# Kernel tuning notes

Measured on AMD Instinct MI355X. Metric: run time of the kernel, lower is better.

Reference implementation:

```python
import jax, jax.numpy as jnp
import numpy as np

B, P, G, CIN, COUT, WD, K3 = 4, 32768, 64, 128, 128, 512, 27
N = B * P


def _build_kernel_map(rng):
    # random sparse occupancy per batch instance on a G^3 grid
    flat = np.stack([rng.choice(G ** 3, size=P, replace=False) for _ in range(B)])  # [B,P]
    b = np.repeat(np.arange(B), P).astype(np.int64)
    f = flat.reshape(-1).astype(np.int64)
    x = f // (G * G); y = (f // G) % G; z = f % G
    keys = b * (G ** 3) + f
    order = np.argsort(keys); skeys = keys[order]
    offsets = [(dx, dy, dz) for dx in (-1, 0, 1) for dy in (-1, 0, 1) for dz in (-1, 0, 1)]
    in_idx = np.full((K3, N), N, np.int32)   # N is a dummy (zero-feature) row
    out_idx = np.full((K3, N), N, np.int32)  # N is a dummy (discarded) output row
    for k, (dx, dy, dz) in enumerate(offsets):
        nx, ny, nz = x + dx, y + dy, z + dz
        inb = (nx >= 0) & (nx < G) & (ny >= 0) & (ny < G) & (nz >= 0) & (nz < G)
        nkey = b * (G ** 3) + (nx * G + ny) * G + nz
        pos = np.clip(np.searchsorted(skeys, nkey), 0, N - 1)
        found = inb & (skeys[pos] == nkey)
        cnt = int(found.sum())
        in_idx[k, :cnt] = order[pos[found]]
        out_idx[k, :cnt] = np.nonzero(found)[0]
    return b.astype(np.int32), in_idx, out_idx


def setup_inputs() -> dict:
    rng = np.random.default_rng(0)
    batch_idx, in_idx, out_idx = _build_kernel_map(rng)
    key = jax.random.key(0)
    k1, k2, k3, k4 = jax.random.split(key, 4)
    return {
        "x_feat": jax.random.normal(k1, (N, CIN), jnp.float32),
        "w": jax.random.normal(k2, (B, WD), jnp.float32),
        "affine_weight": jax.random.normal(k3, (CIN, WD), jnp.float32),
        "affine_bias": jnp.ones((CIN,), jnp.float32),  # bias_init=1
        "conv_weight": jax.random.normal(k4, (COUT, CIN, 3, 3, 3), jnp.float32),
        "conv_bias": jnp.zeros((COUT,), jnp.float32),
        "magnitude_ema": jnp.ones((), jnp.float32),
        "batch_idx": jnp.asarray(batch_idx),
        "in_idx": jnp.asarray(in_idx),
        "out_idx": jnp.asarray(out_idx),
    }


def reference(x_feat, w, affine_weight, affine_bias, conv_weight, conv_bias,
              magnitude_ema, batch_idx, in_idx, out_idx):
    n, cin = x_feat.shape
    cout = conv_weight.shape[0]
    # affine: FullyConnectedLayer with weight_gain = 1/sqrt(in_features), bias_init=1
    styles = w @ (affine_weight * (1.0 / np.sqrt(affine_weight.shape[1]))).T + affine_bias  # [B,Cin]
    # demodulate pre-normalization
    wn = conv_weight * jax.lax.rsqrt(jnp.mean(jnp.square(conv_weight), axis=(1, 2, 3, 4), keepdims=True))
    sn = styles * jax.lax.rsqrt(jnp.mean(jnp.square(styles)))
    sw = wn[None] * sn[:, None, :, None, None, None]              # [B,Cout,Cin,3,3,3]
    dcoefs = jax.lax.rsqrt(jnp.sum(jnp.square(sw), axis=(2, 3, 4, 5)) + 1e-8)  # [B,Cout]
    # non-fused modconv: per-point style modulation (index_select by batch column)
    xmod = x_feat * sn[batch_idx]                                 # [N,Cin]
    xpad = jnp.concatenate([xmod, jnp.zeros((1, cin), xmod.dtype)], axis=0)
    # sparse conv: gather -> GEMM -> scatter-add per kernel offset
    wk = jnp.transpose(wn.reshape(cout, cin, K3), (2, 1, 0))      # [27,Cin,Cout]
    out = jnp.zeros((n + 1, cout), x_feat.dtype)
    for k in range(K3):
        out = out.at[out_idx[k]].add(xpad[in_idx[k]] @ wk[k])
    out = out[:n]
    out = out * dcoefs[batch_idx]                                 # demodulation per point
    out = out * jax.lax.rsqrt(magnitude_ema)                      # input_gain
    # fused bias + leaky relu + gain + clamp
    out = out + conv_bias
    out = jnp.where(out < 0, 0.2 * out, out) * np.sqrt(2.0)
    return jnp.clip(out, -256.0, 256.0)
```

## Files before the change

### kernel.cpp

```cpp
#include <hip/hip_runtime.h>
#include <stdint.h>

#define NPTS 131072
#define CINC 128
#define COUTC 128
#define WDIM 512
#define K3 27

typedef float f32x4 __attribute__((ext_vector_type(4)));
typedef __bf16 bf16x8 __attribute__((ext_vector_type(8)));

#define GLOAD_LDS16(g, l) \
  __builtin_amdgcn_global_load_lds((const __attribute__((address_space(1))) void*)(g), \
                                   (__attribute__((address_space(3))) void*)(l), 16, 0, 0)

__device__ __forceinline__ unsigned short f2bf(float x){
  union { float f; uint32_t u; } v; v.f = x;
  uint32_t u = v.u;
  uint32_t r = (u + 0x7fffu + ((u >> 16) & 1u)) >> 16;
  return (unsigned short)r;
}

__global__ void k_styles_dot(const float* __restrict__ w, const float* __restrict__ aw,
                             const float* __restrict__ ab, float* __restrict__ styles){
  int wave = threadIdx.x >> 6, lane = threadIdx.x & 63;
  int blk = blockIdx.x * 4 + wave;
  int b = blk >> 7, c = blk & 127;
  const float4* wr = (const float4*)(w + b * WDIM);
  const float4* ar = (const float4*)(aw + c * WDIM);
  float4 w0 = wr[lane * 2], w1 = wr[lane * 2 + 1];
  float4 a0 = ar[lane * 2], a1 = ar[lane * 2 + 1];
  float s = w0.x * a0.x + w0.y * a0.y + w0.z * a0.z + w0.w * a0.w
          + w1.x * a1.x + w1.y * a1.y + w1.z * a1.z + w1.w * a1.w;
  for (int off = 32; off > 0; off >>= 1) s += __shfl_down(s, off, 64);
  if (lane == 0) styles[blk] = s * 0.04419417382415922f + ab[c];
}

__global__ void k_snorm(const float* __restrict__ styles, float* __restrict__ sn){
  __shared__ float red[512];
  int t = threadIdx.x;
  float s = styles[t];
  red[t] = s * s;
  __syncthreads();
  for (int off = 256; off > 0; off >>= 1){
    if (t < off) red[t] += red[t + off];
    __syncthreads();
  }
  sn[t] = s * rsqrtf(red[0] * (1.0f / 512.0f));
}

__global__ void k_prep_w(const float* __restrict__ cw, float* __restrict__ wnorm,
                         float* __restrict__ vmat, unsigned short* __restrict__ bpack){
  __shared__ float red[128];
  int co = blockIdx.x, cin = threadIdx.x;
  const float* p = cw + co * 3456 + cin * 27;
  float r[27];
  float v = 0.f;
  #pragma unroll
  for (int k = 0; k < 27; k++){ r[k] = p[k]; v += r[k] * r[k]; }
  vmat[co * 128 + cin] = v;
  red[cin] = v;
  __syncthreads();
  for (int off = 64; off > 0; off >>= 1){
    if (cin < off) red[cin] += red[cin + off];
    __syncthreads();
  }
  float wn_s = rsqrtf(red[0] * (1.0f / 3456.0f));
  if (cin == 0) wnorm[co] = wn_s;
  int grp = co >> 4, m = co & 15;
  int kk = cin >> 5, q = (cin >> 3) & 3, j = cin & 7;
  #pragma unroll
  for (int k = 0; k < 27; k++){
    int idx = ((k * 32 + kk * 8 + grp) * 64 + q * 16 + m) * 8 + j;
    bpack[idx] = f2bf(r[k] * wn_s);
  }
}

__global__ void k_dcoefs2(const float* __restrict__ vmat, const float* __restrict__ sn,
                          const float* __restrict__ wnorm, const float* __restrict__ mag,
                          float* __restrict__ dco2){
  int wave = threadIdx.x >> 6, lane = threadIdx.x & 63;
  int pair = blockIdx.x * 8 + wave;
  int b = pair >> 7, co = pair & 127;
  float s0 = sn[b * 128 + lane], s1 = sn[b * 128 + 64 + lane];
  float sum = vmat[co * 128 + lane] * s0 * s0 + vmat[co * 128 + 64 + lane] * s1 * s1;
  for (int off = 32; off > 0; off >>= 1) sum += __shfl_down(sum, off, 64);
  if (lane == 0){
    float wn = wnorm[co];
    dco2[pair] = rsqrtf(sum * wn * wn + 1e-8f) * rsqrtf(mag[0]);
  }
}

__global__ void k_xmod(const float* __restrict__ x, const float* __restrict__ sn,
                       const int* __restrict__ bidx, unsigned short* __restrict__ xpad){
  int gid = blockIdx.x * 256 + threadIdx.x;
  const int total = (NPTS + 1) * 32;
  if (gid >= total) return;
  int n = gid >> 5;
  int c4 = (gid & 31) * 4;
  unsigned short o0, o1, o2, o3;
  if (n < NPTS){
    int b = bidx[n];
    float4 xv = *(const float4*)(x + (size_t)n * CINC + c4);
    float4 sv = *(const float4*)(sn + b * CINC + c4);
    o0 = f2bf(xv.x * sv.x); o1 = f2bf(xv.y * sv.y);
    o2 = f2bf(xv.z * sv.z); o3 = f2bf(xv.w * sv.w);
  } else { o0 = o1 = o2 = o3 = 0; }
  *(ushort4*)(xpad + (size_t)n * CINC + c4) = make_ushort4(o0, o1, o2, o3);
}

__global__ void k_invinit(int* __restrict__ invT){
  int j = blockIdx.x * 256 + threadIdx.x;
  int k = blockIdx.y;
  invT[k * NPTS + j] = NPTS;
}

__global__ void k_invscat(const int* __restrict__ out_idx, const int* __restrict__ in_idx,
                          int* __restrict__ invT){
  int j = blockIdx.x * 256 + threadIdx.x;
  int k = blockIdx.y;
  int o = out_idx[k * NPTS + j];
  if (o < NPTS) invT[k * NPTS + o] = in_idx[k * NPTS + j];
}

__global__ __launch_bounds__(512, 4) void k_conv(
    const unsigned short* __restrict__ xpad,
    const unsigned short* __restrict__ bpack,
    const int* __restrict__ invT,
    const float* __restrict__ dco2,
    const float* __restrict__ cbias,
    const int* __restrict__ bidx,
    float* __restrict__ out){
  __shared__ __align__(16) unsigned short Ash[2 * 128 * 128];
  int t = threadIdx.x;
  int wave = t >> 6, lane = t & 63;
  int wm = wave >> 1, wn = wave & 1;
  int q = lane >> 4, m16 = lane & 15;
  int base_pt = blockIdx.x * 128;

  f32x4 acc[2][4];
  #pragma unroll
  for (int i = 0; i < 2; i++)
    #pragma unroll
    for (int j = 0; j < 4; j++) acc[i][j] = (f32x4){0.f, 0.f, 0.f, 0.f};

  auto prefetch = [&](int k, int bufsel){
    const int* invk = invT + k * NPTS + base_pt;
    unsigned short* Ab = Ash + bufsel * (128 * 128);
    #pragma unroll
    for (int i = 0; i < 4; i++){
      int chunk = i * 512 + t;
      int row = chunk >> 4, c = chunk & 15;
      int inv = invk[row];
      const unsigned short* src = xpad + (size_t)inv * CINC + ((c ^ row) & 15) * 8;
      GLOAD_LDS16(src, Ab + chunk * 8);
    }
  };

  prefetch(0, 0);
  for (int k = 0; k < K3; k++){
    __syncthreads();
    if (k + 1 < K3) prefetch(k + 1, (k + 1) & 1);
    const unsigned short* Ab = Ash + (k & 1) * (128 * 128);
    const unsigned short* Bg = bpack + k * 16384;
    #pragma unroll
    for (int kk = 0; kk < 4; kk++){
      int cA = ((kk * 4 + q) ^ m16) & 15;
      bf16x8 a0 = *(const bf16x8*)(Ab + (wm * 32 + m16) * 128 + cA * 8);
      bf16x8 a1 = *(const bf16x8*)(Ab + (wm * 32 + 16 + m16) * 128 + cA * 8);
      #pragma unroll
      for (int jn = 0; jn < 4; jn++){
        bf16x8 b = *(const bf16x8*)(Bg + ((kk * 8 + wn * 4 + jn) * 64 + lane) * 8);
        acc[0][jn] = __builtin_amdgcn_mfma_f32_16x16x32_bf16(a0, b, acc[0][jn], 0, 0, 0);
        acc[1][jn] = __builtin_amdgcn_mfma_f32_16x16x32_bf16(a1, b, acc[1][jn], 0, 0, 0);
      }
    }
  }

  const float S2 = 1.41421356237309515f;
  #pragma unroll
  for (int i = 0; i < 2; i++){
    #pragma unroll
    for (int r = 0; r < 4; r++){
      int row = wm * 32 + i * 16 + q * 4 + r;
      int n = base_pt + row;
      int b = bidx[n];
      const float* dc = dco2 + b * COUTC;
      float* orow = out + (size_t)n * COUTC;
      #pragma unroll
      for (int jn = 0; jn < 4; jn++){
        int col = wn * 64 + jn * 16 + m16;
        float v = acc[i][jn][r] * dc[col] + cbias[col];
        v = (v < 0.f ? 0.2f * v : v) * S2;
        v = fminf(fmaxf(v, -256.f), 256.f);
        orow[col] = v;
      }
    }
  }
}

extern "C" void kernel_launch(void* const* d_in, const int* in_sizes, int n_in,
                              void* d_out, int out_size, void* d_ws, size_t ws_size,
                              hipStream_t stream){
  const float* x   = (const float*)d_in[0];
  const float* w   = (const float*)d_in[1];
  const float* aw  = (const float*)d_in[2];
  const float* ab  = (const float*)d_in[3];
  const float* cw  = (const float*)d_in[4];
  const float* cb  = (const float*)d_in[5];
  const float* mag = (const float*)d_in[6];
  const int* bidx    = (const int*)d_in[7];
  const int* in_idx  = (const int*)d_in[8];
  const int* out_idx = (const int*)d_in[9];
  float* out = (float*)d_out;
  char* ws = (char*)d_ws;

  float* styles = (float*)(ws + 0);
  float* sn     = (float*)(ws + 2048);
  float* wnorm  = (float*)(ws + 4096);
  float* dco2   = (float*)(ws + 4608);
  float* vmat   = (float*)(ws + 8192);
  unsigned short* bpack = (unsigned short*)(ws + 73728);
  unsigned short* xpad  = (unsigned short*)(ws + 958464);
  int* invT     = (int*)(ws + 34513152);

  k_prep_w<<<128, 128, 0, stream>>>(cw, wnorm, vmat, bpack);
  k_styles_dot<<<128, 256, 0, stream>>>(w, aw, ab, styles);
  k_snorm<<<1, 512, 0, stream>>>(styles, sn);
  k_dcoefs2<<<64, 512, 0, stream>>>(vmat, sn, wnorm, mag, dco2);
  k_xmod<<<16385, 256, 0, stream>>>(x, sn, bidx, xpad);
  dim3 gi(512, 27);
  k_invinit<<<gi, 256, 0, stream>>>(invT);
  k_invscat<<<gi, 256, 0, stream>>>(out_idx, in_idx, invT);
  k_conv<<<1024, 512, 0, stream>>>(xpad, bpack, invT, dco2, cb, bidx, out);
}
```

Before: 322.9 us.

## Replace inverse-map gather conv with compacted per-tap GEMM plus atomic scatter

```diff
diff --git a/kernel.cpp b/kernel.cpp
--- a/kernel.cpp
+++ b/kernel.cpp
@@ -36,7 +36,9 @@
   if (lane == 0) styles[blk] = s * 0.04419417382415922f + ab[c];
 }
 
-__global__ void k_snorm(const float* __restrict__ styles, float* __restrict__ sn){
+__global__ void k_sn_dco(const float* __restrict__ styles, const float* __restrict__ vmat,
+                         const float* __restrict__ wnorm, const float* __restrict__ mag,
+                         float* __restrict__ sn, float* __restrict__ dco2){
   __shared__ float red[512];
   int t = threadIdx.x;
   float s = styles[t];
@@ -46,7 +48,18 @@
     if (t < off) red[t] += red[t + off];
     __syncthreads();
   }
-  sn[t] = s * rsqrtf(red[0] * (1.0f / 512.0f));
+  float rs = rsqrtf(red[0] * (1.0f / 512.0f));
+  if (blockIdx.x == 0) sn[t] = s * rs;
+  int wave = t >> 6, lane = t & 63;
+  int pair = blockIdx.x * 8 + wave;
+  int b = pair >> 7, co = pair & 127;
+  float s0 = styles[b * 128 + lane] * rs, s1 = styles[b * 128 + 64 + lane] * rs;
+  float sum = vmat[co * 128 + lane] * s0 * s0 + vmat[co * 128 + 64 + lane] * s1 * s1;
+  for (int off = 32; off > 0; off >>= 1) sum += __shfl_down(sum, off, 64);
+  if (lane == 0){
+    float wn = wnorm[co];
+    dco2[pair] = rsqrtf(sum * wn * wn + 1e-8f) * rsqrtf(mag[0]);
+  }
 }
 
 __global__ void k_prep_w(const float* __restrict__ cw, float* __restrict__ wnorm,
@@ -73,21 +86,6 @@
   for (int k = 0; k < 27; k++){
     int idx = ((k * 32 + kk * 8 + grp) * 64 + q * 16 + m) * 8 + j;
     bpack[idx] = f2bf(r[k] * wn_s);
-  }
-}
-
-__global__ void k_dcoefs2(const float* __restrict__ vmat, const float* __restrict__ sn,
-                          const float* __restrict__ wnorm, const float* __restrict__ mag,
-                          float* __restrict__ dco2){
-  int wave = threadIdx.x >> 6, lane = threadIdx.x & 63;
-  int pair = blockIdx.x * 8 + wave;
-  int b = pair >> 7, co = pair & 127;
-  float s0 = sn[b * 128 + lane], s1 = sn[b * 128 + 64 + lane];
-  float sum = vmat[co * 128 + lane] * s0 * s0 + vmat[co * 128 + 64 + lane] * s1 * s1;
-  for (int off = 32; off > 0; off >>= 1) sum += __shfl_down(sum, off, 64);
-  if (lane == 0){
-    float wn = wnorm[co];
-    dco2[pair] = rsqrtf(sum * wn * wn + 1e-8f) * rsqrtf(mag[0]);
   }
 }
 
@@ -109,34 +107,24 @@
   *(ushort4*)(xpad + (size_t)n * CINC + c4) = make_ushort4(o0, o1, o2, o3);
 }
 
-__global__ void k_invinit(int* __restrict__ invT){
-  int j = blockIdx.x * 256 + threadIdx.x;
-  int k = blockIdx.y;
-  invT[k * NPTS + j] = NPTS;
-}
-
-__global__ void k_invscat(const int* __restrict__ out_idx, const int* __restrict__ in_idx,
-                          int* __restrict__ invT){
-  int j = blockIdx.x * 256 + threadIdx.x;
-  int k = blockIdx.y;
-  int o = out_idx[k * NPTS + j];
-  if (o < NPTS) invT[k * NPTS + o] = in_idx[k * NPTS + j];
-}
-
-__global__ __launch_bounds__(512, 4) void k_conv(
+__global__ __launch_bounds__(512, 4) void k_center(
     const unsigned short* __restrict__ xpad,
     const unsigned short* __restrict__ bpack,
-    const int* __restrict__ invT,
-    const float* __restrict__ dco2,
-    const float* __restrict__ cbias,
-    const int* __restrict__ bidx,
     float* __restrict__ out){
-  __shared__ __align__(16) unsigned short Ash[2 * 128 * 128];
+  __shared__ __align__(16) unsigned short Ash[128 * 128];
   int t = threadIdx.x;
   int wave = t >> 6, lane = t & 63;
   int wm = wave >> 1, wn = wave & 1;
   int q = lane >> 4, m16 = lane & 15;
-  int base_pt = blockIdx.x * 128;
+  int base = blockIdx.x * 128;
+
+  #pragma unroll
+  for (int i = 0; i < 4; i++){
+    int chunk = i * 512 + t;
+    int row = chunk >> 4, c = chunk & 15;
+    const unsigned short* src = xpad + (size_t)(base + row) * CINC + ((c ^ row) & 15) * 8;
+    GLOAD_LDS16(src, Ash + chunk * 8);
+  }
 
   f32x4 acc[2][4];
   #pragma unroll
@@ -144,59 +132,114 @@
     #pragma unroll
     for (int j = 0; j < 4; j++) acc[i][j] = (f32x4){0.f, 0.f, 0.f, 0.f};
 
-  auto prefetch = [&](int k, int bufsel){
-    const int* invk = invT + k * NPTS + base_pt;
-    unsigned short* Ab = Ash + bufsel * (128 * 128);
-    #pragma unroll
-    for (int i = 0; i < 4; i++){
-      int chunk = i * 512 + t;
-      int row = chunk >> 4, c = chunk & 15;
-      int inv = invk[row];
-      const unsigned short* src = xpad + (size_t)inv * CINC + ((c ^ row) & 15) * 8;
-      GLOAD_LDS16(src, Ab + chunk * 8);
-    }
-  };
-
-  prefetch(0, 0);
-  for (int k = 0; k < K3; k++){
-    __syncthreads();
-    if (k + 1 < K3) prefetch(k + 1, (k + 1) & 1);
-    const unsigned short* Ab = Ash + (k & 1) * (128 * 128);
-    const unsigned short* Bg = bpack + k * 16384;
-    #pragma unroll
-    for (int kk = 0; kk < 4; kk++){
-      int cA = ((kk * 4 + q) ^ m16) & 15;
-      bf16x8 a0 = *(const bf16x8*)(Ab + (wm * 32 + m16) * 128 + cA * 8);
-      bf16x8 a1 = *(const bf16x8*)(Ab + (wm * 32 + 16 + m16) * 128 + cA * 8);
-      #pragma unroll
-      for (int jn = 0; jn < 4; jn++){
-        bf16x8 b = *(const bf16x8*)(Bg + ((kk * 8 + wn * 4 + jn) * 64 + lane) * 8);
-        acc[0][jn] = __builtin_amdgcn_mfma_f32_16x16x32_bf16(a0, b, acc[0][jn], 0, 0, 0);
-        acc[1][jn] = __builtin_amdgcn_mfma_f32_16x16x32_bf16(a1, b, acc[1][jn], 0, 0, 0);
-      }
-    }
-  }
-
-  const float S2 = 1.41421356237309515f;
-  #pragma unroll
-  for (int i = 0; i < 2; i++){
+  __syncthreads();
+  const unsigned short* Bg = bpack + 13 * 16384;
+  #pragma unroll
+  for (int kk = 0; kk < 4; kk++){
+    int cA = ((kk * 4 + q) ^ m16) & 15;
+    bf16x8 a0 = *(const bf16x8*)(Ash + (wm * 32 + m16) * 128 + cA * 8);
+    bf16x8 a1 = *(const bf16x8*)(Ash + (wm * 32 + 16 + m16) * 128 + cA * 8);
+    #pragma unroll
+    for (int jn = 0; jn < 4; jn++){
+      bf16x8 b = *(const bf16x8*)(Bg + ((kk * 8 + wn * 4 + jn) * 64 + lane) * 8);
+      acc[0][jn] = __builtin_amdgcn_mfma_f32_16x16x32_bf16(a0, b, acc[0][jn], 0, 0, 0);
+      acc[1][jn] = __builtin_amdgcn_mfma_f32_16x16x32_bf16(a1, b, acc[1][jn], 0, 0, 0);
+    }
+  }
+
+  #pragma unroll
+  for (int i = 0; i < 2; i++)
     #pragma unroll
     for (int r = 0; r < 4; r++){
       int row = wm * 32 + i * 16 + q * 4 + r;
-      int n = base_pt + row;
-      int b = bidx[n];
-      const float* dc = dco2 + b * COUTC;
-      float* orow = out + (size_t)n * COUTC;
+      float* orow = out + (size_t)(base + row) * COUTC;
       #pragma unroll
-      for (int jn = 0; jn < 4; jn++){
-        int col = wn * 64 + jn * 16 + m16;
-        float v = acc[i][jn][r] * dc[col] + cbias[col];
-        v = (v < 0.f ? 0.2f * v : v) * S2;
-        v = fminf(fmaxf(v, -256.f), 256.f);
-        orow[col] = v;
+      for (int jn = 0; jn < 4; jn++)
+        orow[wn * 64 + jn * 16 + m16] = acc[i][jn][r];
+    }
+}
+
+__global__ __launch_bounds__(512, 4) void k_taps(
+    const unsigned short* __restrict__ xpad,
+    const unsigned short* __restrict__ bpack,
+    const int* __restrict__ in_idx,
+    const int* __restrict__ out_idx,
+    float* __restrict__ out){
+  int u = blockIdx.x;
+  int kt = u >> 10;
+  int tile = u & 1023;
+  int k = kt + (kt >= 13);
+  const int* ink  = in_idx  + k * NPTS + tile * 128;
+  const int* outk = out_idx + k * NPTS + tile * 128;
+  if (outk[0] >= NPTS) return;
+
+  __shared__ __align__(16) unsigned short Ash[128 * 128];
+  int t = threadIdx.x;
+  int wave = t >> 6, lane = t & 63;
+  int wm = wave >> 1, wn = wave & 1;
+  int q = lane >> 4, m16 = lane & 15;
+
+  #pragma unroll
+  for (int i = 0; i < 4; i++){
+    int chunk = i * 512 + t;
+    int row = chunk >> 4, c = chunk & 15;
+    int inv = ink[row];
+    const unsigned short* src = xpad + (size_t)inv * CINC + ((c ^ row) & 15) * 8;
+    GLOAD_LDS16(src, Ash + chunk * 8);
+  }
+
+  f32x4 acc[2][4];
+  #pragma unroll
+  for (int i = 0; i < 2; i++)
+    #pragma unroll
+    for (int j = 0; j < 4; j++) acc[i][j] = (f32x4){0.f, 0.f, 0.f, 0.f};
+
+  __syncthreads();
+  const unsigned short* Bg = bpack + k * 16384;
+  #pragma unroll
+  for (int kk = 0; kk < 4; kk++){
+    int cA = ((kk * 4 + q) ^ m16) & 15;
+    bf16x8 a0 = *(const bf16x8*)(Ash + (wm * 32 + m16) * 128 + cA * 8);
+    bf16x8 a1 = *(const bf16x8*)(Ash + (wm * 32 + 16 + m16) * 128 + cA * 8);
+    #pragma unroll
+    for (int jn = 0; jn < 4; jn++){
+      bf16x8 b = *(const bf16x8*)(Bg + ((kk * 8 + wn * 4 + jn) * 64 + lane) * 8);
+      acc[0][jn] = __builtin_amdgcn_mfma_f32_16x16x32_bf16(a0, b, acc[0][jn], 0, 0, 0);
+      acc[1][jn] = __builtin_amdgcn_mfma_f32_16x16x32_bf16(a1, b, acc[1][jn], 0, 0, 0);
+    }
+  }
+
+  #pragma unroll
+  for (int i = 0; i < 2; i++)
+    #pragma unroll
+    for (int r = 0; r < 4; r++){
+      int row = wm * 32 + i * 16 + q * 4 + r;
+      int o = outk[row];
+      if (o < NPTS){
+        float* orow = out + (size_t)o * COUTC;
+        #pragma unroll
+        for (int jn = 0; jn < 4; jn++)
+          unsafeAtomicAdd(&orow[wn * 64 + jn * 16 + m16], acc[i][jn][r]);
       }
     }
-  }
+}
+
+__global__ void k_epi(float* __restrict__ out, const float* __restrict__ dco2,
+                      const float* __restrict__ cbias, const int* __restrict__ bidx){
+  int gid = blockIdx.x * 256 + threadIdx.x;
+  if (gid >= NPTS * 32) return;
+  int n = gid >> 5;
+  int c4 = (gid & 31) * 4;
+  int b = bidx[n];
+  float4 v = *(float4*)(out + (size_t)n * COUTC + c4);
+  float4 d = *(const float4*)(dco2 + b * COUTC + c4);
+  float4 bi = *(const float4*)(cbias + c4);
+  const float S2 = 1.41421356237309515f;
+  float r0 = v.x * d.x + bi.x; r0 = (r0 < 0.f ? 0.2f * r0 : r0) * S2; r0 = fminf(fmaxf(r0, -256.f), 256.f);
+  float r1 = v.y * d.y + bi.y; r1 = (r1 < 0.f ? 0.2f * r1 : r1) * S2; r1 = fminf(fmaxf(r1, -256.f), 256.f);
+  float r2 = v.z * d.z + bi.z; r2 = (r2 < 0.f ? 0.2f * r2 : r2) * S2; r2 = fminf(fmaxf(r2, -256.f), 256.f);
+  float r3 = v.w * d.w + bi.w; r3 = (r3 < 0.f ? 0.2f * r3 : r3) * S2; r3 = fminf(fmaxf(r3, -256.f), 256.f);
+  *(float4*)(out + (size_t)n * COUTC + c4) = make_float4(r0, r1, r2, r3);
 }
 
 extern "C" void kernel_launch(void* const* d_in, const int* in_sizes, int n_in,
@@ -222,15 +265,12 @@
   float* vmat   = (float*)(ws + 8192);
   unsigned short* bpack = (unsigned short*)(ws + 73728);
   unsigned short* xpad  = (unsigned short*)(ws + 958464);
-  int* invT     = (int*)(ws + 34513152);
 
   k_prep_w<<<128, 128, 0, stream>>>(cw, wnorm, vmat, bpack);
   k_styles_dot<<<128, 256, 0, stream>>>(w, aw, ab, styles);
-  k_snorm<<<1, 512, 0, stream>>>(styles, sn);
-  k_dcoefs2<<<64, 512, 0, stream>>>(vmat, sn, wnorm, mag, dco2);
+  k_sn_dco<<<64, 512, 0, stream>>>(styles, vmat, wnorm, mag, sn, dco2);
   k_xmod<<<16385, 256, 0, stream>>>(x, sn, bidx, xpad);
-  dim3 gi(512, 27);
-  k_invinit<<<gi, 256, 0, stream>>>(invT);
-  k_invscat<<<gi, 256, 0, stream>>>(out_idx, in_idx, invT);
-  k_conv<<<1024, 512, 0, stream>>>(xpad, bpack, invT, dco2, cb, bidx, out);
-}
+  k_center<<<1024, 512, 0, stream>>>(xpad, bpack, out);
+  k_taps<<<26 * 1024, 512, 0, stream>>>(xpad, bpack, in_idx, out_idx, out);
+  k_epi<<<16384, 256, 0, stream>>>(out, dco2, cb, bidx);
+}
```

Measured after the change: 362.0 us. 12.1% more time.

## Replace dense inverse-map conv with sparse range-based gather and LDS atomic scatter

Applied to the files above, without the earlier changes.

```diff
diff --git a/kernel.cpp b/kernel.cpp
--- a/kernel.cpp
+++ b/kernel.cpp
@@ -6,13 +6,10 @@
 #define COUTC 128
 #define WDIM 512
 #define K3 27
+#define NTILES 1024
 
 typedef float f32x4 __attribute__((ext_vector_type(4)));
 typedef __bf16 bf16x8 __attribute__((ext_vector_type(8)));
-
-#define GLOAD_LDS16(g, l) \
-  __builtin_amdgcn_global_load_lds((const __attribute__((address_space(1))) void*)(g), \
-                                   (__attribute__((address_space(3))) void*)(l), 16, 0, 0)
 
 __device__ __forceinline__ unsigned short f2bf(float x){
   union { float f; uint32_t u; } v; v.f = x;
@@ -36,7 +33,9 @@
   if (lane == 0) styles[blk] = s * 0.04419417382415922f + ab[c];
 }
 
-__global__ void k_snorm(const float* __restrict__ styles, float* __restrict__ sn){
+__global__ void k_sn_dco(const float* __restrict__ styles, const float* __restrict__ vmat,
+                         const float* __restrict__ wnorm, const float* __restrict__ mag,
+                         float* __restrict__ sn, float* __restrict__ dco2){
   __shared__ float red[512];
   int t = threadIdx.x;
   float s = styles[t];
@@ -46,7 +45,18 @@
     if (t < off) red[t] += red[t + off];
     __syncthreads();
   }
-  sn[t] = s * rsqrtf(red[0] * (1.0f / 512.0f));
+  float rs = rsqrtf(red[0] * (1.0f / 512.0f));
+  if (blockIdx.x == 0) sn[t] = s * rs;
+  int wave = t >> 6, lane = t & 63;
+  int pair = blockIdx.x * 8 + wave;
+  int b = pair >> 7, co = pair & 127;
+  float s0 = styles[b * 128 + lane] * rs, s1 = styles[b * 128 + 64 + lane] * rs;
+  float sum = vmat[co * 128 + lane] * s0 * s0 + vmat[co * 128 + 64 + lane] * s1 * s1;
+  for (int off = 32; off > 0; off >>= 1) sum += __shfl_down(sum, off, 64);
+  if (lane == 0){
+    float wn = wnorm[co];
+    dco2[pair] = rsqrtf(sum * wn * wn + 1e-8f) * rsqrtf(mag[0]);
+  }
 }
 
 __global__ void k_prep_w(const float* __restrict__ cw, float* __restrict__ wnorm,
@@ -73,21 +83,6 @@
   for (int k = 0; k < 27; k++){
     int idx = ((k * 32 + kk * 8 + grp) * 64 + q * 16 + m) * 8 + j;
     bpack[idx] = f2bf(r[k] * wn_s);
-  }
-}
-
-__global__ void k_dcoefs2(const float* __restrict__ vmat, const float* __restrict__ sn,
-                          const float* __restrict__ wnorm, const float* __restrict__ mag,
-                          float* __restrict__ dco2){
-  int wave = threadIdx.x >> 6, lane = threadIdx.x & 63;
-  int pair = blockIdx.x * 8 + wave;
-  int b = pair >> 7, co = pair & 127;
-  float s0 = sn[b * 128 + lane], s1 = sn[b * 128 + 64 + lane];
-  float sum = vmat[co * 128 + lane] * s0 * s0 + vmat[co * 128 + 64 + lane] * s1 * s1;
-  for (int off = 32; off > 0; off >>= 1) sum += __shfl_down(sum, off, 64);
-  if (lane == 0){
-    float wn = wnorm[co];
-    dco2[pair] = rsqrtf(sum * wn * wn + 1e-8f) * rsqrtf(mag[0]);
   }
 }
 
@@ -109,93 +104,105 @@
   *(ushort4*)(xpad + (size_t)n * CINC + c4) = make_ushort4(o0, o1, o2, o3);
 }
 
-__global__ void k_invinit(int* __restrict__ invT){
-  int j = blockIdx.x * 256 + threadIdx.x;
-  int k = blockIdx.y;
-  invT[k * NPTS + j] = NPTS;
-}
-
-__global__ void k_invscat(const int* __restrict__ out_idx, const int* __restrict__ in_idx,
-                          int* __restrict__ invT){
-  int j = blockIdx.x * 256 + threadIdx.x;
-  int k = blockIdx.y;
-  int o = out_idx[k * NPTS + j];
-  if (o < NPTS) invT[k * NPTS + o] = in_idx[k * NPTS + j];
-}
-
-__global__ __launch_bounds__(512, 4) void k_conv(
+__global__ void k_ranges(const int* __restrict__ out_idx, int* __restrict__ R){
+  int gid = blockIdx.x * 256 + threadIdx.x;
+  if (gid >= K3 * (NTILES + 1)) return;
+  int k = gid / (NTILES + 1), t = gid - k * (NTILES + 1);
+  int target = t * 128;
+  const int* lst = out_idx + k * NPTS;
+  int lo = 0, hi = NPTS;
+  while (lo < hi){ int mid = (lo + hi) >> 1; if (lst[mid] < target) lo = mid + 1; else hi = mid; }
+  R[gid] = lo;
+}
+
+__device__ __forceinline__ int caddr(int row, int col){
+  return row * 128 + ((((col) >> 2) + row & 31) << 2) + (col & 3);
+}
+
+__global__ __launch_bounds__(512, 4) void k_out(
     const unsigned short* __restrict__ xpad,
     const unsigned short* __restrict__ bpack,
-    const int* __restrict__ invT,
+    const int* __restrict__ in_idx,
+    const int* __restrict__ out_idx,
+    const int* __restrict__ R,
     const float* __restrict__ dco2,
     const float* __restrict__ cbias,
     const int* __restrict__ bidx,
     float* __restrict__ out){
-  __shared__ __align__(16) unsigned short Ash[2 * 128 * 128];
+  __shared__ float Csh[128 * 128];
   int t = threadIdx.x;
   int wave = t >> 6, lane = t & 63;
-  int wm = wave >> 1, wn = wave & 1;
-  int q = lane >> 4, m16 = lane & 15;
-  int base_pt = blockIdx.x * 128;
-
-  f32x4 acc[2][4];
-  #pragma unroll
-  for (int i = 0; i < 2; i++)
-    #pragma unroll
-    for (int j = 0; j < 4; j++) acc[i][j] = (f32x4){0.f, 0.f, 0.f, 0.f};
-
-  auto prefetch = [&](int k, int bufsel){
-    const int* invk = invT + k * NPTS + base_pt;
-    unsigned short* Ab = Ash + bufsel * (128 * 128);
-    #pragma unroll
-    for (int i = 0; i < 4; i++){
-      int chunk = i * 512 + t;
-      int row = chunk >> 4, c = chunk & 15;
-      int inv = invk[row];
-      const unsigned short* src = xpad + (size_t)inv * CINC + ((c ^ row) & 15) * 8;
-      GLOAD_LDS16(src, Ab + chunk * 8);
-    }
-  };
-
-  prefetch(0, 0);
+  int m16 = lane & 15, q = lane >> 4;
+  int tile = blockIdx.x;
+  int tbase = tile * 128;
+
+  #pragma unroll
+  for (int i = 0; i < 8; i++)
+    *(f32x4*)(Csh + i * 2048 + t * 4) = (f32x4){0.f, 0.f, 0.f, 0.f};
+  __syncthreads();
+
+  int tc = 0;
   for (int k = 0; k < K3; k++){
-    __syncthreads();
-    if (k + 1 < K3) prefetch(k + 1, (k + 1) & 1);
-    const unsigned short* Ab = Ash + (k & 1) * (128 * 128);
+    int lo = R[k * (NTILES + 1) + tile];
+    int hi = R[k * (NTILES + 1) + tile + 1];
+    int groups = (hi - lo + 15) >> 4;
     const unsigned short* Bg = bpack + k * 16384;
-    #pragma unroll
-    for (int kk = 0; kk < 4; kk++){
-      int cA = ((kk * 4 + q) ^ m16) & 15;
-      bf16x8 a0 = *(const bf16x8*)(Ab + (wm * 32 + m16) * 128 + cA * 8);
-      bf16x8 a1 = *(const bf16x8*)(Ab + (wm * 32 + 16 + m16) * 128 + cA * 8);
+    const int* ink  = in_idx  + k * NPTS;
+    const int* outk = out_idx + k * NPTS;
+    for (int g = 0; g < groups; g++, tc++){
+      if ((tc & 7) != wave) continue;
+      int e = lo + g * 16 + m16;
+      int in = (e < hi) ? ink[e] : NPTS;
+      const unsigned short* arow = xpad + (size_t)in * CINC + q * 8;
+      bf16x8 a0 = *(const bf16x8*)(arow);
+      bf16x8 a1 = *(const bf16x8*)(arow + 32);
+      bf16x8 a2 = *(const bf16x8*)(arow + 64);
+      bf16x8 a3 = *(const bf16x8*)(arow + 96);
+      f32x4 acc[8];
       #pragma unroll
-      for (int jn = 0; jn < 4; jn++){
-        bf16x8 b = *(const bf16x8*)(Bg + ((kk * 8 + wn * 4 + jn) * 64 + lane) * 8);
-        acc[0][jn] = __builtin_amdgcn_mfma_f32_16x16x32_bf16(a0, b, acc[0][jn], 0, 0, 0);
-        acc[1][jn] = __builtin_amdgcn_mfma_f32_16x16x32_bf16(a1, b, acc[1][jn], 0, 0, 0);
+      for (int j = 0; j < 8; j++) acc[j] = (f32x4){0.f, 0.f, 0.f, 0.f};
+      #pragma unroll
+      for (int grp = 0; grp < 8; grp++){
+        bf16x8 b0 = *(const bf16x8*)(Bg + ((0 * 8 + grp) * 64 + lane) * 8);
+        bf16x8 b1 = *(const bf16x8*)(Bg + ((1 * 8 + grp) * 64 + lane) * 8);
+        bf16x8 b2 = *(const bf16x8*)(Bg + ((2 * 8 + grp) * 64 + lane) * 8);
+        bf16x8 b3 = *(const bf16x8*)(Bg + ((3 * 8 + grp) * 64 + lane) * 8);
+        acc[grp] = __builtin_amdgcn_mfma_f32_16x16x32_bf16(a0, b0, acc[grp], 0, 0, 0);
+        acc[grp] = __builtin_amdgcn_mfma_f32_16x16x32_bf16(a1, b1, acc[grp], 0, 0, 0);
+        acc[grp] = __builtin_amdgcn_mfma_f32_16x16x32_bf16(a2, b2, acc[grp], 0, 0, 0);
+        acc[grp] = __builtin_amdgcn_mfma_f32_16x16x32_bf16(a3, b3, acc[grp], 0, 0, 0);
+      }
+      #pragma unroll
+      for (int r = 0; r < 4; r++){
+        int ee = lo + g * 16 + q * 4 + r;
+        if (ee < hi){
+          int orow = outk[ee] - tbase;
+          #pragma unroll
+          for (int grp = 0; grp < 8; grp++)
+            unsafeAtomicAdd(&Csh[caddr(orow, grp * 16 + m16)], acc[grp][r]);
+        }
       }
     }
   }
-
+  __syncthreads();
+
+  int row = t >> 2, cb = (t & 3) * 32;
+  int n = tbase + row;
+  int b = bidx[n];
+  const float* dc = dco2 + b * COUTC;
+  float* orow = out + (size_t)n * COUTC;
   const float S2 = 1.41421356237309515f;
   #pragma unroll
-  for (int i = 0; i < 2; i++){
-    #pragma unroll
-    for (int r = 0; r < 4; r++){
-      int row = wm * 32 + i * 16 + q * 4 + r;
-      int n = base_pt + row;
-      int b = bidx[n];
-      const float* dc = dco2 + b * COUTC;
-      float* orow = out + (size_t)n * COUTC;
-      #pragma unroll
-      for (int jn = 0; jn < 4; jn++){
-        int col = wn * 64 + jn * 16 + m16;
-        float v = acc[i][jn][r] * dc[col] + cbias[col];
-        v = (v < 0.f ? 0.2f * v : v) * S2;
-        v = fminf(fmaxf(v, -256.f), 256.f);
-        orow[col] = v;
-      }
-    }
+  for (int i = 0; i < 8; i++){
+    int c = cb + i * 4;
+    f32x4 v = *(const f32x4*)(Csh + caddr(row, c));
+    float4 d = *(const float4*)(dc + c);
+    float4 bi = *(const float4*)(cbias + c);
+    float r0 = v.x * d.x + bi.x; r0 = (r0 < 0.f ? 0.2f * r0 : r0) * S2; r0 = fminf(fmaxf(r0, -256.f), 256.f);
+    float r1 = v.y * d.y + bi.y; r1 = (r1 < 0.f ? 0.2f * r1 : r1) * S2; r1 = fminf(fmaxf(r1, -256.f), 256.f);
+    float r2 = v.z * d.z + bi.z; r2 = (r2 < 0.f ? 0.2f * r2 : r2) * S2; r2 = fminf(fmaxf(r2, -256.f), 256.f);
+    float r3 = v.w * d.w + bi.w; r3 = (r3 < 0.f ? 0.2f * r3 : r3) * S2; r3 = fminf(fmaxf(r3, -256.f), 256.f);
+    *(float4*)(orow + c) = make_float4(r0, r1, r2, r3);
   }
 }
 
@@ -222,15 +229,12 @@
   float* vmat   = (float*)(ws + 8192);
   unsigned short* bpack = (unsigned short*)(ws + 73728);
   unsigned short* xpad  = (unsigned short*)(ws + 958464);
-  int* invT     = (int*)(ws + 34513152);
+  int* R        = (int*)(ws + 34513152);
 
   k_prep_w<<<128, 128, 0, stream>>>(cw, wnorm, vmat, bpack);
   k_styles_dot<<<128, 256, 0, stream>>>(w, aw, ab, styles);
-  k_snorm<<<1, 512, 0, stream>>>(styles, sn);
-  k_dcoefs2<<<64, 512, 0, stream>>>(vmat, sn, wnorm, mag, dco2);
+  k_sn_dco<<<64, 512, 0, stream>>>(styles, vmat, wnorm, mag, sn, dco2);
   k_xmod<<<16385, 256, 0, stream>>>(x, sn, bidx, xpad);
-  dim3 gi(512, 27);
-  k_invinit<<<gi, 256, 0, stream>>>(invT);
-  k_invscat<<<gi, 256, 0, stream>>>(out_idx, in_idx, invT);
-  k_conv<<<1024, 512, 0, stream>>>(xpad, bpack, invT, dco2, cb, bidx, out);
-}
+  k_ranges<<<109, 256, 0, stream>>>(out_idx, R);
+  k_out<<<NTILES, 512, 0, stream>>>(xpad, bpack, in_idx, out_idx, R, dco2, cb, bidx, out);
+}
```

Measured after the change: 550.0 us. +70.3%, slower.
